# Kernel optimization log

Hardware: AMD Instinct MI355X
Metric: run time of the kernel (lower is better)

The kernel has to match this reference:

```python
import jax, jax.numpy as jnp
import numpy as np

N = 100000
E = 1200000
D_IN = 64
D_OUT = 64


def setup_inputs() -> dict:
    key = jax.random.key(0)
    ks = jax.random.split(key, 12)
    s = 1.0 / np.sqrt(D_IN)
    return {
        "n_in_feats": jax.random.normal(ks[0], (N, D_IN), dtype=jnp.float32),
        "r_feats": jax.random.normal(ks[1], (D_IN,), dtype=jnp.float32),
        "src": jax.random.randint(ks[2], (E,), 0, N, dtype=jnp.int32),
        "dst": jax.random.randint(ks[3], (E,), 0, N, dtype=jnp.int32),
        "W_O": jax.random.normal(ks[4], (D_OUT, D_IN), dtype=jnp.float32) * s,
        "b_O": jax.random.normal(ks[5], (D_OUT,), dtype=jnp.float32) * s,
        "W_I": jax.random.normal(ks[6], (D_OUT, D_IN), dtype=jnp.float32) * s,
        "b_I": jax.random.normal(ks[7], (D_OUT,), dtype=jnp.float32) * s,
        "W_S": jax.random.normal(ks[8], (D_OUT, D_IN), dtype=jnp.float32) * s,
        "b_S": jax.random.normal(ks[9], (D_OUT,), dtype=jnp.float32) * s,
        "W_R": jax.random.normal(ks[10], (D_OUT, D_IN), dtype=jnp.float32) * s,
        "b_R": jax.random.normal(ks[11], (D_OUT,), dtype=jnp.float32) * s,
    }


def reference(n_in_feats, r_feats, src, dst, W_O, b_O, W_I, b_I, W_S, b_S, W_R, b_R):
    # comp_fn == 'sub': fn.u_sub_v composes src node feats with dst node feats
    comp_h = n_in_feats[src] - n_in_feats[dst]          # [E, D_IN]
    half = comp_h.shape[0] // 2
    # split linear transforms: first half (original edges) -> W_O, second -> W_I
    h_O = comp_h[:half] @ W_O.T + b_O                    # [E/2, D_OUT]
    h_I = comp_h[half:] @ W_I.T + b_I                    # [E/2, D_OUT]
    new_comp_h = jnp.concatenate([h_O, h_I], axis=0)     # [E, D_OUT]
    # copy_e + sum: scatter edge messages to destination nodes
    comp_edge = jax.ops.segment_sum(new_comp_h, dst, num_segments=n_in_feats.shape[0])
    # self loop path
    comp_h_s = n_in_feats - r_feats                      # broadcast [N, D_IN]
    n_out_feats = comp_h_s @ W_S.T + b_S + comp_edge     # [N, D_OUT]
    r_out_feats = r_feats @ W_R.T + b_R                  # [D_OUT]
    # batchnorm=False, dropout=0, activation=None -> identity
    return n_out_feats, r_out_feats
```

## Files before the change

### kernel.cpp

```cpp
#include <hip/hip_runtime.h>


#define DF 64
#define BCAP 2560
#define CPAD 16
#define NBMAX 1024
#define SCHUNK 4096
typedef _Float16 f16;
typedef f16 f16x8 __attribute__((ext_vector_type(8)));
typedef f16 f16x4 __attribute__((ext_vector_type(4)));
typedef f16 f16x2 __attribute__((ext_vector_type(2)));
typedef float f32x4 __attribute__((ext_vector_type(4)));

__global__ __launch_bounds__(256) void prep_dense(const float* __restrict__ x,
                                                  const float* __restrict__ r,
                                                  f16* __restrict__ A,
                                                  f16* __restrict__ ytab,
                                                  const float* __restrict__ W_S,
                                                  const float* __restrict__ W_O,
                                                  const float* __restrict__ W_I,
                                                  f16* __restrict__ Wf, int N) {
    int t = blockIdx.x * 256 + threadIdx.x;
    int ny = N * 32;
    if (t < ny) {
        int v = t >> 5, k = (t & 31) * 2;
        float y0 = x[(size_t)v * DF + k]     - r[k];
        float y1 = x[(size_t)v * DF + k + 1] - r[k + 1];
        f16x2 p = {(f16)y0, (f16)y1};
        *(f16x2*)(A + (size_t)v * 192 + k) = p;
        if (ytab) *(f16x2*)(ytab + (size_t)v * 64 + k) = p;
    }
    if (t < 6144) {
        int w = t / 2048;
        int i = (t % 2048) * 2;
        const float* W = (w == 0) ? W_S : (w == 1) ? W_O : W_I;
        f16x2 p = {(f16)W[i], (f16)W[i + 1]};
        *(f16x2*)(Wf + w * 4096 + i) = p;
    }
}

__global__ __launch_bounds__(512) void scatter_edges(const int* __restrict__ src,
                                                     const int* __restrict__ dst,
                                                     int* __restrict__ cur,
                                                     unsigned int* __restrict__ pairBuf,
                                                     int E, int half, int NB) {
    __shared__ int cnt[NBMAX];
    int t = threadIdx.x;
    int e0 = blockIdx.x * SCHUNK;
    int n = E - e0; if (n > SCHUNK) n = SCHUNK;
    for (int k = t; k < NBMAX; k += 512) cnt[k] = 0;
    __syncthreads();

    unsigned int ent[SCHUNK / 512];
    int bk[SCHUNK / 512];
    #pragma unroll
    for (int i = 0; i < SCHUNK / 512; i++) {
        int idx = t + i * 512;
        bk[i] = -1;
        if (idx < n) {
            int e = e0 + idx;
            int s = __builtin_nontemporal_load(src + e);
            int d = __builtin_nontemporal_load(dst + e);
            int key = (d << 1) | (e >= half ? 1 : 0);
            int b = key >> 8;
            ent[i] = (unsigned int)s | ((unsigned int)(key & 255) << 24);
            bk[i] = b;
            atomicAdd(&cnt[b], 1);
        }
    }
    __syncthreads();

    for (int k = t; k < NB; k += 512) {
        int c = cnt[k];
        cnt[k] = (c > 0) ? atomicAdd(&cur[k * CPAD], c) : 0;
    }
    __syncthreads();

    #pragma unroll
    for (int i = 0; i < SCHUNK / 512; i++) {
        if (bk[i] >= 0) {
            int pos = atomicAdd(&cnt[bk[i]], 1);
            if (pos < BCAP)
                pairBuf[(size_t)bk[i] * BCAP + pos] = ent[i];
        }
    }
}

__global__ __launch_bounds__(256) void bucket_sort(unsigned int* __restrict__ pairBuf,
                                                   const int* __restrict__ cur,
                                                   int* __restrict__ deg,
                                                   int* __restrict__ off, int M) {
    __shared__ unsigned int P[2048];
    __shared__ int cnt[256];
    __shared__ int pos[256];
    int b = blockIdx.x;
    int t = threadIdx.x;
    cnt[t] = 0;
    __syncthreads();
    int n = cur[b * CPAD];
    if (n > 2048) n = 2048;
    const unsigned int* seg = pairBuf + (size_t)b * BCAP;
    for (int i = t; i < n; i += 256) {
        unsigned int p = seg[i];
        P[i] = p;
        atomicAdd(&cnt[p >> 24], 1);
    }
    __syncthreads();
    int v = cnt[t];
    pos[t] = v;
    __syncthreads();
    #pragma unroll
    for (int s = 1; s < 256; s <<= 1) {
        int u = (t >= s) ? pos[t - s] : 0;
        __syncthreads();
        pos[t] += u;
        __syncthreads();
    }
    int incl = pos[t];
    int key = (b << 8) + t;
    if (key < M) {
        deg[key] = v;
        off[key] = b * BCAP + incl;
    }
    __syncthreads();
    pos[t] = incl - v;
    __syncthreads();
    unsigned int* outb = pairBuf + (size_t)b * BCAP;
    for (int i = t; i < n; i += 256) {
        unsigned int p = P[i];
        int lk = p >> 24;
        int loc = atomicAdd(&pos[lk], 1);
        outb[loc] = p & 0xFFFFFFu;
    }
}

__global__ __launch_bounds__(256) void gather_sum(const f16* __restrict__ Y,
                                                  int ystride,
                                                  f16* __restrict__ A,
                                                  const int* __restrict__ deg,
                                                  const int* __restrict__ off,
                                                  const unsigned int* __restrict__ srcList,
                                                  int N) {
    int p = (blockIdx.x * 256 + threadIdx.x) >> 6;
    int lane = threadIdx.x & 63;
    int v0 = 2 * p, v1 = 2 * p + 1;
    if (v0 >= N) return;
    const int g = lane >> 4, q = lane & 15;
    bool hasV1 = (v1 < N);
    int dO0 = deg[4 * p], dI0 = deg[4 * p + 1];
    int dO1 = hasV1 ? deg[4 * p + 2] : 0;
    int dI1 = hasV1 ? deg[4 * p + 3] : 0;
    int s = off[4 * p] - dO0;
    int t1 = s + dO0, t2 = t1 + dI0, t3 = t2 + dO1;
    int end = t3 + dI1;

    const f16x2 zz = {(f16)0.f, (f16)0.f};
    f16x2 aA0 = zz, aA1 = zz, a10 = zz, a11 = zz,
          a20 = zz, a21 = zz, a30 = zz, a31 = zz;

    int e = s;
    for (; e + 8 <= end; e += 8) {
        int eA = e + g, eB = e + g + 4;
        int iA = (int)srcList[eA];
        int iB = (int)srcList[eB];
        const f16x2* pa = (const f16x2*)(Y + (size_t)iA * ystride + 4 * q);
        const f16x2* pb = (const f16x2*)(Y + (size_t)iB * ystride + 4 * q);
        f16x2 va0 = pa[0], va1 = pa[1];
        f16x2 vb0 = pb[0], vb1 = pb[1];
        aA0 += va0; aA1 += va1;
        a10 += (eA >= t1) ? va0 : zz;  a11 += (eA >= t1) ? va1 : zz;
        a20 += (eA >= t2) ? va0 : zz;  a21 += (eA >= t2) ? va1 : zz;
        a30 += (eA >= t3) ? va0 : zz;  a31 += (eA >= t3) ? va1 : zz;
        aA0 += vb0; aA1 += vb1;
        a10 += (eB >= t1) ? vb0 : zz;  a11 += (eB >= t1) ? vb1 : zz;
        a20 += (eB >= t2) ? vb0 : zz;  a21 += (eB >= t2) ? vb1 : zz;
        a30 += (eB >= t3) ? vb0 : zz;  a31 += (eB >= t3) ? vb1 : zz;
    }
    if (e < end) {
        int eA = e + g, eB = e + g + 4;
        bool inA = (eA < end), inB = (eB < end);
        int iA = inA ? (int)srcList[eA] : 0;
        int iB = inB ? (int)srcList[eB] : 0;
        const f16x2* pa = (const f16x2*)(Y + (size_t)iA * ystride + 4 * q);
        const f16x2* pb = (const f16x2*)(Y + (size_t)iB * ystride + 4 * q);
        f16x2 va0 = pa[0], va1 = pa[1];
        f16x2 vb0 = pb[0], vb1 = pb[1];
        aA0 += inA ? va0 : zz; aA1 += inA ? va1 : zz;
        a10 += (inA && eA >= t1) ? va0 : zz;  a11 += (inA && eA >= t1) ? va1 : zz;
        a20 += (inA && eA >= t2) ? va0 : zz;  a21 += (inA && eA >= t2) ? va1 : zz;
        a30 += (inA && eA >= t3) ? va0 : zz;  a31 += (inA && eA >= t3) ? va1 : zz;
        aA0 += inB ? vb0 : zz; aA1 += inB ? vb1 : zz;
        a10 += (inB && eB >= t1) ? vb0 : zz;  a11 += (inB && eB >= t1) ? vb1 : zz;
        a20 += (inB && eB >= t2) ? vb0 : zz;  a21 += (inB && eB >= t2) ? vb1 : zz;
        a30 += (inB && eB >= t3) ? vb0 : zz;  a31 += (inB && eB >= t3) ? vb1 : zz;
    }

    f16x2 acc[8] = {aA0, aA1, a10, a11, a20, a21, a30, a31};
    #pragma unroll
    for (int i = 0; i < 8; i++) {
        int w = __builtin_bit_cast(int, acc[i]);
        f16x2 u16 = __builtin_bit_cast(f16x2, __shfl_xor(w, 16, 64));
        acc[i] += u16;
        w = __builtin_bit_cast(int, acc[i]);
        f16x2 u32 = __builtin_bit_cast(f16x2, __shfl_xor(w, 32, 64));
        acc[i] += u32;
    }
    f16x2 d0l = acc[0] - acc[2], d0h = acc[1] - acc[3];
    f16x2 d1l = acc[2] - acc[4], d1h = acc[3] - acc[5];
    f16x2 d2l = acc[4] - acc[6], d2h = acc[5] - acc[7];
    f16x2 d3l = acc[6],          d3h = acc[7];
    f16x2 wl01 = (g == 0) ? d0l : d1l, wh01 = (g == 0) ? d0h : d1h;
    f16x2 wl23 = (g == 2) ? d2l : d3l, wh23 = (g == 2) ? d2h : d3h;
    f16x2 wl = (g < 2) ? wl01 : wl23,  wh = (g < 2) ? wh01 : wh23;

    int vtgt = (g < 2) ? v0 : v1;
    int voff = (g & 1) ? 128 : 64;
    float d01 = (g == 0) ? (float)dO0 : (float)dI0;
    float d23 = (g == 2) ? (float)dO1 : (float)dI1;
    float dd = (g < 2) ? d01 : d23;
    if (vtgt < N) {
        const f16x2* yp = (const f16x2*)(Y + (size_t)vtgt * ystride + 4 * q);
        f16x2 y0 = yp[0], y1 = yp[1];
        f16x4 res;
        res[0] = (f16)((float)wl[0] - dd * (float)y0[0]);
        res[1] = (f16)((float)wl[1] - dd * (float)y0[1]);
        res[2] = (f16)((float)wh[0] - dd * (float)y1[0]);
        res[3] = (f16)((float)wh[1] - dd * (float)y1[1]);
        *(f16x4*)(A + (size_t)vtgt * 192 + voff + 4 * q) = res;
    }
}

__global__ __launch_bounds__(256) void gemv_mfma(const f16* __restrict__ A,
                                                 const f16* __restrict__ Wf,
                                                 const int* __restrict__ deg,
                                                 const float* __restrict__ b_O,
                                                 const float* __restrict__ b_I,
                                                 const float* __restrict__ b_S,
                                                 float* __restrict__ out,
                                                 int N, int nTiles) {
    int gw = (blockIdx.x * 256 + threadIdx.x) >> 6;
    int nw = gridDim.x * 4;
    const int lane = threadIdx.x & 63;
    const int mlane = lane & 15;
    const int koff = (lane >> 4) * 8;

    for (int tile = gw; tile < nTiles; tile += nw) {
        const int vbase = tile * 16;
        int va = vbase + mlane; if (va >= N) va = N - 1;
        const f16* arow = A + (size_t)va * 192 + koff;
        f16x8 af[6];
        #pragma unroll
        for (int s = 0; s < 6; s++) af[s] = *(const f16x8*)(arow + s * 32);

        f32x4 accs[4];
        #pragma unroll
        for (int c = 0; c < 4; c++) {
            f32x4 acc = {0.f, 0.f, 0.f, 0.f};
            #pragma unroll
            for (int s = 0; s < 6; s++) {
                int k = s * 32 + koff;
                const f16* bp = Wf + (k >> 6) * 4096 + (c * 16 + mlane) * 64 + (k & 63);
                f16x8 bf = *(const f16x8*)bp;
                acc = __builtin_amdgcn_mfma_f32_16x16x32_f16(af[s], bf, acc, 0, 0, 0);
            }
            accs[c] = acc;
        }

        const int mrow0 = (lane >> 4) * 4;
        #pragma unroll
        for (int reg = 0; reg < 4; reg++) {
            int v = vbase + mrow0 + reg;
            if (v >= N) continue;
            float cO = (float)deg[2 * v], cI = (float)deg[2 * v + 1];
            #pragma unroll
            for (int c = 0; c < 4; c++) {
                int j = c * 16 + mlane;
                out[(size_t)v * DF + j] = accs[c][reg] + b_S[j] + cO * b_O[j] + cI * b_I[j];
            }
        }
    }
}

__global__ void r_transform(const float* __restrict__ r,
                            const float* __restrict__ W_R,
                            const float* __restrict__ b_R,
                            float* __restrict__ out, int N) {
    int j = threadIdx.x;
    float s = b_R[j];
    #pragma unroll 16
    for (int k = 0; k < 64; k++) s += r[k] * W_R[j * 64 + k];
    out[(size_t)N * DF + j] = s;
}

extern "C" void kernel_launch(void* const* d_in, const int* in_sizes, int n_in,
                              void* d_out, int out_size, void* d_ws, size_t ws_size,
                              hipStream_t stream) {
    const float* x   = (const float*)d_in[0];
    const float* r   = (const float*)d_in[1];
    const int*   src = (const int*)d_in[2];
    const int*   dst = (const int*)d_in[3];
    const float* W_O = (const float*)d_in[4];
    const float* b_O = (const float*)d_in[5];
    const float* W_I = (const float*)d_in[6];
    const float* b_I = (const float*)d_in[7];
    const float* W_S = (const float*)d_in[8];
    const float* b_S = (const float*)d_in[9];
    const float* W_R = (const float*)d_in[10];
    const float* b_R = (const float*)d_in[11];
    float* out = (float*)d_out;

    const int N = in_sizes[0] / DF;
    const int E = in_sizes[2];
    const int half = E / 2;
    const int M = 2 * N;
    const int NB = (M + 255) >> 8;

    f16* A  = (f16*)d_ws;
    f16* Wf = A + (size_t)N * 192;
    int* deg = (int*)(Wf + 3 * 4096);
    int* off = deg + M;
    int* cur = off + M;
    unsigned int* pairBuf = (unsigned int*)(cur + (size_t)NB * CPAD);
    f16* ytab = (f16*)(pairBuf + (size_t)NB * BCAP);
    size_t need = (size_t)((char*)(ytab + (size_t)N * 64) - (char*)d_ws);
    const bool useYtab = (ws_size >= need);
    f16* ytabArg = useYtab ? ytab : nullptr;
    const f16* Y = useYtab ? ytab : A;
    const int ystride = useYtab ? 64 : 192;

    hipMemsetAsync(cur, 0, (size_t)NB * CPAD * sizeof(int), stream);

    scatter_edges<<<(E + SCHUNK - 1) / SCHUNK, 512, 0, stream>>>(src, dst, cur,
                                                                 pairBuf, E, half, NB);
    int nThread = N * 32;
    prep_dense<<<(nThread + 255) / 256, 256, 0, stream>>>(x, r, A, ytabArg,
                                                          W_S, W_O, W_I, Wf, N);
    bucket_sort<<<NB, 256, 0, stream>>>(pairBuf, cur, deg, off, M);

    int nPairs = (N + 1) / 2;
    int gsBlocks = (nPairs + 3) / 4;
    gather_sum<<<gsBlocks, 256, 0, stream>>>(Y, ystride, A, deg, off, pairBuf, N);

    int nTiles = (N + 15) / 16;
    gemv_mfma<<<1024, 256, 0, stream>>>(A, Wf, deg, b_O, b_I, b_S, out, N, nTiles);
    r_transform<<<1, 64, 0, stream>>>(r, W_R, b_R, out, N);
}
```

Before: 200.0 us.

## Fuse scatter with prep, bucket sort with gather, and r_transform into gemv

Merges the edge scatter and dense prep into one launch that splits blocks by role, and fuses the per-bucket sort with the neighbour gather-sum. The sorted source list now stays in LDS and is read from there rather than written back to global memory, and the global off array is dropped. The r-transform moves into the first block of the gemv kernel. The aim is to cut launch count and a global round trip of the sorted edge list, at the cost of 512-thread blocks for the gather and less parallelism per node pair.

```diff
diff --git a/kernel.cpp b/kernel.cpp
--- a/kernel.cpp
+++ b/kernel.cpp
@@ -12,221 +12,215 @@
 typedef f16 f16x2 __attribute__((ext_vector_type(2)));
 typedef float f32x4 __attribute__((ext_vector_type(4)));
 
-__global__ __launch_bounds__(256) void prep_dense(const float* __restrict__ x,
-                                                  const float* __restrict__ r,
-                                                  f16* __restrict__ A,
-                                                  f16* __restrict__ ytab,
-                                                  const float* __restrict__ W_S,
-                                                  const float* __restrict__ W_O,
-                                                  const float* __restrict__ W_I,
-                                                  f16* __restrict__ Wf, int N) {
-    int t = blockIdx.x * 256 + threadIdx.x;
-    int ny = N * 32;
-    if (t < ny) {
-        int v = t >> 5, k = (t & 31) * 2;
-        float y0 = x[(size_t)v * DF + k]     - r[k];
-        float y1 = x[(size_t)v * DF + k + 1] - r[k + 1];
-        f16x2 p = {(f16)y0, (f16)y1};
-        *(f16x2*)(A + (size_t)v * 192 + k) = p;
-        if (ytab) *(f16x2*)(ytab + (size_t)v * 64 + k) = p;
-    }
-    if (t < 6144) {
-        int w = t / 2048;
-        int i = (t % 2048) * 2;
-        const float* W = (w == 0) ? W_S : (w == 1) ? W_O : W_I;
-        f16x2 p = {(f16)W[i], (f16)W[i + 1]};
-        *(f16x2*)(Wf + w * 4096 + i) = p;
+__global__ __launch_bounds__(512) void scatter_prep(
+    const int* __restrict__ src, const int* __restrict__ dst,
+    int* __restrict__ cur, unsigned int* __restrict__ pairBuf,
+    int E, int half, int NB, int SB,
+    const float* __restrict__ x, const float* __restrict__ r,
+    f16* __restrict__ A, f16* __restrict__ ytab,
+    const float* __restrict__ W_S, const float* __restrict__ W_O,
+    const float* __restrict__ W_I, f16* __restrict__ Wf, int N) {
+    int t = threadIdx.x;
+    if ((int)blockIdx.x < SB) {
+        __shared__ int cnt[NBMAX];
+        int e0 = blockIdx.x * SCHUNK;
+        int n = E - e0; if (n > SCHUNK) n = SCHUNK;
+        for (int k = t; k < NBMAX; k += 512) cnt[k] = 0;
+        __syncthreads();
+
+        unsigned int ent[SCHUNK / 512];
+        int bk[SCHUNK / 512];
+        #pragma unroll
+        for (int i = 0; i < SCHUNK / 512; i++) {
+            int idx = t + i * 512;
+            bk[i] = -1;
+            if (idx < n) {
+                int e = e0 + idx;
+                int s = __builtin_nontemporal_load(src + e);
+                int d = __builtin_nontemporal_load(dst + e);
+                int key = (d << 1) | (e >= half ? 1 : 0);
+                int b = key >> 8;
+                ent[i] = (unsigned int)s | ((unsigned int)(key & 255) << 24);
+                bk[i] = b;
+                atomicAdd(&cnt[b], 1);
+            }
+        }
+        __syncthreads();
+        for (int k = t; k < NB; k += 512) {
+            int c = cnt[k];
+            cnt[k] = (c > 0) ? atomicAdd(&cur[k * CPAD], c) : 0;
+        }
+        __syncthreads();
+        #pragma unroll
+        for (int i = 0; i < SCHUNK / 512; i++) {
+            if (bk[i] >= 0) {
+                int pos = atomicAdd(&cnt[bk[i]], 1);
+                if (pos < BCAP)
+                    pairBuf[(size_t)bk[i] * BCAP + pos] = ent[i];
+            }
+        }
+    } else {
+        int tt = ((int)blockIdx.x - SB) * 512 + t;
+        int ny = N * 32;
+        if (tt < ny) {
+            int v = tt >> 5, k = (tt & 31) * 2;
+            float y0 = x[(size_t)v * DF + k]     - r[k];
+            float y1 = x[(size_t)v * DF + k + 1] - r[k + 1];
+            f16x2 p = {(f16)y0, (f16)y1};
+            *(f16x2*)(A + (size_t)v * 192 + k) = p;
+            if (ytab) *(f16x2*)(ytab + (size_t)v * 64 + k) = p;
+        }
+        if (tt < 6144) {
+            int w = tt / 2048;
+            int i = (tt % 2048) * 2;
+            const float* W = (w == 0) ? W_S : (w == 1) ? W_O : W_I;
+            f16x2 p = {(f16)W[i], (f16)W[i + 1]};
+            *(f16x2*)(Wf + w * 4096 + i) = p;
+        }
     }
 }
 
-__global__ __launch_bounds__(512) void scatter_edges(const int* __restrict__ src,
-                                                     const int* __restrict__ dst,
-                                                     int* __restrict__ cur,
-                                                     unsigned int* __restrict__ pairBuf,
-                                                     int E, int half, int NB) {
-    __shared__ int cnt[NBMAX];
-    int t = threadIdx.x;
-    int e0 = blockIdx.x * SCHUNK;
-    int n = E - e0; if (n > SCHUNK) n = SCHUNK;
-    for (int k = t; k < NBMAX; k += 512) cnt[k] = 0;
-    __syncthreads();
-
-    unsigned int ent[SCHUNK / 512];
-    int bk[SCHUNK / 512];
-    #pragma unroll
-    for (int i = 0; i < SCHUNK / 512; i++) {
-        int idx = t + i * 512;
-        bk[i] = -1;
-        if (idx < n) {
-            int e = e0 + idx;
-            int s = __builtin_nontemporal_load(src + e);
-            int d = __builtin_nontemporal_load(dst + e);
-            int key = (d << 1) | (e >= half ? 1 : 0);
-            int b = key >> 8;
-            ent[i] = (unsigned int)s | ((unsigned int)(key & 255) << 24);
-            bk[i] = b;
-            atomicAdd(&cnt[b], 1);
-        }
-    }
-    __syncthreads();
-
-    for (int k = t; k < NB; k += 512) {
-        int c = cnt[k];
-        cnt[k] = (c > 0) ? atomicAdd(&cur[k * CPAD], c) : 0;
-    }
-    __syncthreads();
-
-    #pragma unroll
-    for (int i = 0; i < SCHUNK / 512; i++) {
-        if (bk[i] >= 0) {
-            int pos = atomicAdd(&cnt[bk[i]], 1);
-            if (pos < BCAP)
-                pairBuf[(size_t)bk[i] * BCAP + pos] = ent[i];
-        }
-    }
-}
-
-__global__ __launch_bounds__(256) void bucket_sort(unsigned int* __restrict__ pairBuf,
-                                                   const int* __restrict__ cur,
-                                                   int* __restrict__ deg,
-                                                   int* __restrict__ off, int M) {
-    __shared__ unsigned int P[2048];
+__global__ __launch_bounds__(512) void sort_gather(
+    unsigned int* __restrict__ pairBuf, const int* __restrict__ cur,
+    int* __restrict__ deg,
+    const f16* __restrict__ Y, int ystride, f16* __restrict__ A,
+    int N, int M) {
+    __shared__ unsigned int S[2048 + 8];
     __shared__ int cnt[256];
     __shared__ int pos[256];
-    int b = blockIdx.x;
-    int t = threadIdx.x;
-    cnt[t] = 0;
+    int b = blockIdx.x, t = threadIdx.x;
+    if (t < 256) cnt[t] = 0;
     __syncthreads();
     int n = cur[b * CPAD];
     if (n > 2048) n = 2048;
     const unsigned int* seg = pairBuf + (size_t)b * BCAP;
-    for (int i = t; i < n; i += 256) {
-        unsigned int p = seg[i];
-        P[i] = p;
+    unsigned int ent[4];
+    int ne = 0;
+    for (int idx = t; idx < n; idx += 512) {
+        unsigned int p = seg[idx];
+        ent[ne++] = p;
         atomicAdd(&cnt[p >> 24], 1);
     }
     __syncthreads();
-    int v = cnt[t];
-    pos[t] = v;
+    int v = 0, incl = 0;
+    if (t < 256) { v = cnt[t]; pos[t] = v; }
     __syncthreads();
     #pragma unroll
     for (int s = 1; s < 256; s <<= 1) {
-        int u = (t >= s) ? pos[t - s] : 0;
-        __syncthreads();
-        pos[t] += u;
-        __syncthreads();
-    }
-    int incl = pos[t];
-    int key = (b << 8) + t;
-    if (key < M) {
-        deg[key] = v;
-        off[key] = b * BCAP + incl;
-    }
-    __syncthreads();
-    pos[t] = incl - v;
-    __syncthreads();
-    unsigned int* outb = pairBuf + (size_t)b * BCAP;
-    for (int i = t; i < n; i += 256) {
-        unsigned int p = P[i];
-        int lk = p >> 24;
-        int loc = atomicAdd(&pos[lk], 1);
-        outb[loc] = p & 0xFFFFFFu;
-    }
-}
-
-__global__ __launch_bounds__(256) void gather_sum(const f16* __restrict__ Y,
-                                                  int ystride,
-                                                  f16* __restrict__ A,
-                                                  const int* __restrict__ deg,
-                                                  const int* __restrict__ off,
-                                                  const unsigned int* __restrict__ srcList,
-                                                  int N) {
-    int p = (blockIdx.x * 256 + threadIdx.x) >> 6;
-    int lane = threadIdx.x & 63;
-    int v0 = 2 * p, v1 = 2 * p + 1;
-    if (v0 >= N) return;
+        int u = 0;
+        if (t < 256 && t >= s) u = pos[t - s];
+        __syncthreads();
+        if (t < 256) pos[t] += u;
+        __syncthreads();
+    }
+    if (t < 256) {
+        incl = pos[t];
+        int key = (b << 8) + t;
+        if (key < M) deg[key] = v;
+    }
+    __syncthreads();
+    if (t < 256) pos[t] = incl - v;
+    __syncthreads();
+    for (int j = 0; j < ne; j++) {
+        unsigned int p = ent[j];
+        int loc = atomicAdd(&pos[p >> 24], 1);
+        S[loc] = p & 0xFFFFFFu;
+    }
+    __syncthreads();
+    if (t < 8) S[n + t] = 0;
+    __syncthreads();
+
+    const int wid = t >> 6, lane = t & 63;
     const int g = lane >> 4, q = lane & 15;
-    bool hasV1 = (v1 < N);
-    int dO0 = deg[4 * p], dI0 = deg[4 * p + 1];
-    int dO1 = hasV1 ? deg[4 * p + 2] : 0;
-    int dI1 = hasV1 ? deg[4 * p + 3] : 0;
-    int s = off[4 * p] - dO0;
-    int t1 = s + dO0, t2 = t1 + dI0, t3 = t2 + dO1;
-    int end = t3 + dI1;
-
+    const int vbase = b * 128;
     const f16x2 zz = {(f16)0.f, (f16)0.f};
-    f16x2 aA0 = zz, aA1 = zz, a10 = zz, a11 = zz,
-          a20 = zz, a21 = zz, a30 = zz, a31 = zz;
-
-    int e = s;
-    for (; e + 8 <= end; e += 8) {
-        int eA = e + g, eB = e + g + 4;
-        int iA = (int)srcList[eA];
-        int iB = (int)srcList[eB];
-        const f16x2* pa = (const f16x2*)(Y + (size_t)iA * ystride + 4 * q);
-        const f16x2* pb = (const f16x2*)(Y + (size_t)iB * ystride + 4 * q);
-        f16x2 va0 = pa[0], va1 = pa[1];
-        f16x2 vb0 = pb[0], vb1 = pb[1];
-        aA0 += va0; aA1 += va1;
-        a10 += (eA >= t1) ? va0 : zz;  a11 += (eA >= t1) ? va1 : zz;
-        a20 += (eA >= t2) ? va0 : zz;  a21 += (eA >= t2) ? va1 : zz;
-        a30 += (eA >= t3) ? va0 : zz;  a31 += (eA >= t3) ? va1 : zz;
-        aA0 += vb0; aA1 += vb1;
-        a10 += (eB >= t1) ? vb0 : zz;  a11 += (eB >= t1) ? vb1 : zz;
-        a20 += (eB >= t2) ? vb0 : zz;  a21 += (eB >= t2) ? vb1 : zz;
-        a30 += (eB >= t3) ? vb0 : zz;  a31 += (eB >= t3) ? vb1 : zz;
-    }
-    if (e < end) {
-        int eA = e + g, eB = e + g + 4;
-        bool inA = (eA < end), inB = (eB < end);
-        int iA = inA ? (int)srcList[eA] : 0;
-        int iB = inB ? (int)srcList[eB] : 0;
-        const f16x2* pa = (const f16x2*)(Y + (size_t)iA * ystride + 4 * q);
-        const f16x2* pb = (const f16x2*)(Y + (size_t)iB * ystride + 4 * q);
-        f16x2 va0 = pa[0], va1 = pa[1];
-        f16x2 vb0 = pb[0], vb1 = pb[1];
-        aA0 += inA ? va0 : zz; aA1 += inA ? va1 : zz;
-        a10 += (inA && eA >= t1) ? va0 : zz;  a11 += (inA && eA >= t1) ? va1 : zz;
-        a20 += (inA && eA >= t2) ? va0 : zz;  a21 += (inA && eA >= t2) ? va1 : zz;
-        a30 += (inA && eA >= t3) ? va0 : zz;  a31 += (inA && eA >= t3) ? va1 : zz;
-        aA0 += inB ? vb0 : zz; aA1 += inB ? vb1 : zz;
-        a10 += (inB && eB >= t1) ? vb0 : zz;  a11 += (inB && eB >= t1) ? vb1 : zz;
-        a20 += (inB && eB >= t2) ? vb0 : zz;  a21 += (inB && eB >= t2) ? vb1 : zz;
-        a30 += (inB && eB >= t3) ? vb0 : zz;  a31 += (inB && eB >= t3) ? vb1 : zz;
-    }
-
-    f16x2 acc[8] = {aA0, aA1, a10, a11, a20, a21, a30, a31};
-    #pragma unroll
+
     for (int i = 0; i < 8; i++) {
-        int w = __builtin_bit_cast(int, acc[i]);
-        f16x2 u16 = __builtin_bit_cast(f16x2, __shfl_xor(w, 16, 64));
-        acc[i] += u16;
-        w = __builtin_bit_cast(int, acc[i]);
-        f16x2 u32 = __builtin_bit_cast(f16x2, __shfl_xor(w, 32, 64));
-        acc[i] += u32;
-    }
-    f16x2 d0l = acc[0] - acc[2], d0h = acc[1] - acc[3];
-    f16x2 d1l = acc[2] - acc[4], d1h = acc[3] - acc[5];
-    f16x2 d2l = acc[4] - acc[6], d2h = acc[5] - acc[7];
-    f16x2 d3l = acc[6],          d3h = acc[7];
-    f16x2 wl01 = (g == 0) ? d0l : d1l, wh01 = (g == 0) ? d0h : d1h;
-    f16x2 wl23 = (g == 2) ? d2l : d3l, wh23 = (g == 2) ? d2h : d3h;
-    f16x2 wl = (g < 2) ? wl01 : wl23,  wh = (g < 2) ? wh01 : wh23;
-
-    int vtgt = (g < 2) ? v0 : v1;
-    int voff = (g & 1) ? 128 : 64;
-    float d01 = (g == 0) ? (float)dO0 : (float)dI0;
-    float d23 = (g == 2) ? (float)dO1 : (float)dI1;
-    float dd = (g < 2) ? d01 : d23;
-    if (vtgt < N) {
-        const f16x2* yp = (const f16x2*)(Y + (size_t)vtgt * ystride + 4 * q);
-        f16x2 y0 = yp[0], y1 = yp[1];
-        f16x4 res;
-        res[0] = (f16)((float)wl[0] - dd * (float)y0[0]);
-        res[1] = (f16)((float)wl[1] - dd * (float)y0[1]);
-        res[2] = (f16)((float)wh[0] - dd * (float)y1[0]);
-        res[3] = (f16)((float)wh[1] - dd * (float)y1[1]);
-        *(f16x4*)(A + (size_t)vtgt * 192 + voff + 4 * q) = res;
+        int pp = wid * 8 + i;
+        int v0 = vbase + 2 * pp, v1 = v0 + 1;
+        if (v0 >= N) break;
+        bool hasV1 = (v1 < N);
+        int l0 = 4 * pp;
+        int dO0 = cnt[l0], dI0 = cnt[l0 + 1];
+        int dO1 = hasV1 ? cnt[l0 + 2] : 0;
+        int dI1 = hasV1 ? cnt[l0 + 3] : 0;
+        int s0 = pos[l0] - dO0;
+        int t1 = s0 + dO0, t2 = t1 + dI0, t3 = t2 + dO1;
+        int end = t3 + dI1;
+
+        f16x2 aA0 = zz, aA1 = zz, a10 = zz, a11 = zz,
+              a20 = zz, a21 = zz, a30 = zz, a31 = zz;
+
+        int e = s0;
+        for (; e + 8 <= end; e += 8) {
+            int eA = e + g, eB = e + g + 4;
+            int iA = (int)S[eA];
+            int iB = (int)S[eB];
+            const f16x2* pa = (const f16x2*)(Y + (size_t)iA * ystride + 4 * q);
+            const f16x2* pb = (const f16x2*)(Y + (size_t)iB * ystride + 4 * q);
+            f16x2 va0 = pa[0], va1 = pa[1];
+            f16x2 vb0 = pb[0], vb1 = pb[1];
+            aA0 += va0; aA1 += va1;
+            a10 += (eA >= t1) ? va0 : zz;  a11 += (eA >= t1) ? va1 : zz;
+            a20 += (eA >= t2) ? va0 : zz;  a21 += (eA >= t2) ? va1 : zz;
+            a30 += (eA >= t3) ? va0 : zz;  a31 += (eA >= t3) ? va1 : zz;
+            aA0 += vb0; aA1 += vb1;
+            a10 += (eB >= t1) ? vb0 : zz;  a11 += (eB >= t1) ? vb1 : zz;
+            a20 += (eB >= t2) ? vb0 : zz;  a21 += (eB >= t2) ? vb1 : zz;
+            a30 += (eB >= t3) ? vb0 : zz;  a31 += (eB >= t3) ? vb1 : zz;
+        }
+        if (e < end) {
+            int eA = e + g, eB = e + g + 4;
+            bool inA = (eA < end), inB = (eB < end);
+            int iA = (int)S[eA];
+            int iB = (int)S[eB];
+            const f16x2* pa = (const f16x2*)(Y + (size_t)iA * ystride + 4 * q);
+            const f16x2* pb = (const f16x2*)(Y + (size_t)iB * ystride + 4 * q);
+            f16x2 va0 = pa[0], va1 = pa[1];
+            f16x2 vb0 = pb[0], vb1 = pb[1];
+            aA0 += inA ? va0 : zz; aA1 += inA ? va1 : zz;
+            a10 += (inA && eA >= t1) ? va0 : zz;  a11 += (inA && eA >= t1) ? va1 : zz;
+            a20 += (inA && eA >= t2) ? va0 : zz;  a21 += (inA && eA >= t2) ? va1 : zz;
+            a30 += (inA && eA >= t3) ? va0 : zz;  a31 += (inA && eA >= t3) ? va1 : zz;
+            aA0 += inB ? vb0 : zz; aA1 += inB ? vb1 : zz;
+            a10 += (inB && eB >= t1) ? vb0 : zz;  a11 += (inB && eB >= t1) ? vb1 : zz;
+            a20 += (inB && eB >= t2) ? vb0 : zz;  a21 += (inB && eB >= t2) ? vb1 : zz;
+            a30 += (inB && eB >= t3) ? vb0 : zz;  a31 += (inB && eB >= t3) ? vb1 : zz;
+        }
+
+        f16x2 acc[8] = {aA0, aA1, a10, a11, a20, a21, a30, a31};
+        #pragma unroll
+        for (int k = 0; k < 8; k++) {
+            int w = __builtin_bit_cast(int, acc[k]);
+            f16x2 u16 = __builtin_bit_cast(f16x2, __shfl_xor(w, 16, 64));
+            acc[k] += u16;
+            w = __builtin_bit_cast(int, acc[k]);
+            f16x2 u32 = __builtin_bit_cast(f16x2, __shfl_xor(w, 32, 64));
+            acc[k] += u32;
+        }
+        f16x2 d0l = acc[0] - acc[2], d0h = acc[1] - acc[3];
+        f16x2 d1l = acc[2] - acc[4], d1h = acc[3] - acc[5];
+        f16x2 d2l = acc[4] - acc[6], d2h = acc[5] - acc[7];
+        f16x2 d3l = acc[6],          d3h = acc[7];
+        f16x2 wl01 = (g == 0) ? d0l : d1l, wh01 = (g == 0) ? d0h : d1h;
+        f16x2 wl23 = (g == 2) ? d2l : d3l, wh23 = (g == 2) ? d2h : d3h;
+        f16x2 wl = (g < 2) ? wl01 : wl23,  wh = (g < 2) ? wh01 : wh23;
+
+        int vtgt = (g < 2) ? v0 : v1;
+        int voff = (g & 1) ? 128 : 64;
+        float d01 = (g == 0) ? (float)dO0 : (float)dI0;
+        float d23 = (g == 2) ? (float)dO1 : (float)dI1;
+        float dd = (g < 2) ? d01 : d23;
+        if (vtgt < N) {
+            const f16x2* yp = (const f16x2*)(Y + (size_t)vtgt * ystride + 4 * q);
+            f16x2 y0 = yp[0], y1 = yp[1];
+            f16x4 res;
+            res[0] = (f16)((float)wl[0] - dd * (float)y0[0]);
+            res[1] = (f16)((float)wl[1] - dd * (float)y0[1]);
+            res[2] = (f16)((float)wh[0] - dd * (float)y1[0]);
+            res[3] = (f16)((float)wh[1] - dd * (float)y1[1]);
+            *(f16x4*)(A + (size_t)vtgt * 192 + voff + 4 * q) = res;
+        }
     }
 }
 
@@ -236,8 +230,18 @@
                                                  const float* __restrict__ b_O,
                                                  const float* __restrict__ b_I,
                                                  const float* __restrict__ b_S,
+                                                 const float* __restrict__ r,
+                                                 const float* __restrict__ W_R,
+                                                 const float* __restrict__ b_R,
                                                  float* __restrict__ out,
                                                  int N, int nTiles) {
+    if (blockIdx.x == 0 && threadIdx.x < 64) {
+        int j = threadIdx.x;
+        float s = b_R[j];
+        #pragma unroll 16
+        for (int k = 0; k < 64; k++) s += r[k] * W_R[j * 64 + k];
+        out[(size_t)N * DF + j] = s;
+    }
     int gw = (blockIdx.x * 256 + threadIdx.x) >> 6;
     int nw = gridDim.x * 4;
     const int lane = threadIdx.x & 63;
@@ -279,17 +283,6 @@
             }
         }
     }
-}
-
-__global__ void r_transform(const float* __restrict__ r,
-                            const float* __restrict__ W_R,
-                            const float* __restrict__ b_R,
-                            float* __restrict__ out, int N) {
-    int j = threadIdx.x;
-    float s = b_R[j];
-    #pragma unroll 16
-    for (int k = 0; k < 64; k++) s += r[k] * W_R[j * 64 + k];
-    out[(size_t)N * DF + j] = s;
 }
 
 extern "C" void kernel_launch(void* const* d_in, const int* in_sizes, int n_in,
@@ -318,8 +311,7 @@
     f16* A  = (f16*)d_ws;
     f16* Wf = A + (size_t)N * 192;
     int* deg = (int*)(Wf + 3 * 4096);
-    int* off = deg + M;
-    int* cur = off + M;
+    int* cur = deg + M;
     unsigned int* pairBuf = (unsigned int*)(cur + (size_t)NB * CPAD);
     f16* ytab = (f16*)(pairBuf + (size_t)NB * BCAP);
     size_t need = (size_t)((char*)(ytab + (size_t)N * 64) - (char*)d_ws);
@@ -330,18 +322,16 @@
 
     hipMemsetAsync(cur, 0, (size_t)NB * CPAD * sizeof(int), stream);
 
-    scatter_edges<<<(E + SCHUNK - 1) / SCHUNK, 512, 0, stream>>>(src, dst, cur,
-                                                                 pairBuf, E, half, NB);
-    int nThread = N * 32;
-    prep_dense<<<(nThread + 255) / 256, 256, 0, stream>>>(x, r, A, ytabArg,
-                                                          W_S, W_O, W_I, Wf, N);
-    bucket_sort<<<NB, 256, 0, stream>>>(pairBuf, cur, deg, off, M);
-
-    int nPairs = (N + 1) / 2;
-    int gsBlocks = (nPairs + 3) / 4;
-    gather_sum<<<gsBlocks, 256, 0, stream>>>(Y, ystride, A, deg, off, pairBuf, N);
+    const int SB = (E + SCHUNK - 1) / SCHUNK;
+    const int PB = (N * 32 + 511) / 512;
+    scatter_prep<<<SB + PB, 512, 0, stream>>>(src, dst, cur, pairBuf,
+                                              E, half, NB, SB,
+                                              x, r, A, ytabArg,
+                                              W_S, W_O, W_I, Wf, N);
+
+    sort_gather<<<NB, 512, 0, stream>>>(pairBuf, cur, deg, Y, ystride, A, N, M);
 
     int nTiles = (N + 15) / 16;
-    gemv_mfma<<<1024, 256, 0, stream>>>(A, Wf, deg, b_O, b_I, b_S, out, N, nTiles);
-    r_transform<<<1, 64, 0, stream>>>(r, W_R, b_R, out, N);
+    gemv_mfma<<<1024, 256, 0, stream>>>(A, Wf, deg, b_O, b_I, b_S,
+                                        r, W_R, b_R, out, N, nTiles);
 }
```

Measured after the change: 186.1 us. 1.07x faster.
